# Optimization experiments

Measured on AMD Instinct MI355X. Metric: run time of the kernel, lower is better.

The kernel has to match this reference:

```python
import jax, jax.numpy as jnp
import numpy as np


def setup_inputs() -> dict:
    key = jax.random.key(0)
    k_x, k_w, k_W, k_b, k_idx = jax.random.split(key, 5)
    B, C, N, K, O = 2, 32, 40962, 25, 64
    x = jax.random.normal(k_x, (B, C, N), dtype=jnp.float32)
    neigh_weights = jax.random.uniform(k_w, (N, K, 3), dtype=jnp.float32)
    W = jax.random.normal(k_W, (O, K * C), dtype=jnp.float32) * 0.02
    b = jax.random.normal(k_b, (O,), dtype=jnp.float32) * 0.02
    neigh_indices = jax.random.randint(k_idx, (N, K, 3), 0, N, dtype=jnp.int32)
    return {"x": x, "neigh_weights": neigh_weights, "W": W, "b": b,
            "neigh_indices": neigh_indices}


def reference(x, neigh_weights, W, b, neigh_indices):
    # x: (B, C, N); neigh_indices/neigh_weights: (N, K, 3); W: (O, C*K); b: (O,)
    B, C, N = x.shape
    _, K, _ = neigh_indices.shape
    # Gather neighbor features: (B, C, N, K, 3)
    mat = x[:, :, neigh_indices]
    # Barycentric weighted sum over the 3 triangle vertices -> (B, C, N, K)
    s = jnp.einsum('bcnkt,nkt->bcnk', mat, neigh_weights)
    # Permute to (B, N, C, K) and apply Linear(C*K -> O)
    feat = s.transpose(0, 2, 1, 3).reshape(B * N, C * K)
    out = feat @ W.T + b  # (B*N, O)
    out = out.reshape(B, N, -1).transpose(0, 2, 1)  # (B, O, N)
    return out
```

## Files before the change

### kernel.cpp

```cpp
#include <hip/hip_runtime.h>
#include <hip/hip_fp16.h>

typedef __attribute__((ext_vector_type(8))) _Float16 half8;
typedef __attribute__((ext_vector_type(4))) float f32x4;

union U2H2 { unsigned int u; __half2 h; };

static __device__ __forceinline__ unsigned int pack2h(float a, float b) {
    U2H2 c; c.h = __floats2half2_rn(a, b); return c.u;
}
static __device__ __forceinline__ __half2 u_as_h2(unsigned int u) {
    U2H2 c; c.u = u; return c.h;
}
static __device__ __forceinline__ __half2 hi16(unsigned int u) {
    return u_as_h2(__builtin_amdgcn_perm(u, u, 0x03020302u));
}

#define SWZ(row, slot) \
    ((slot) ^ ((row) & 3) ^ (((row) >> 2) & 3) ^ (((row) >> 5) & 1))

#define LDS_BARRIER()                                                \
    do {                                                             \
        asm volatile("s_waitcnt lgkmcnt(0)" ::: "memory");           \
        __builtin_amdgcn_s_barrier();                                \
        __builtin_amdgcn_sched_barrier(0);                           \
    } while (0)

__global__ __launch_bounds__(256) void prep_all(const float* __restrict__ x,
                                                const float* __restrict__ W,
                                                unsigned short* __restrict__ xth,
                                                unsigned short* __restrict__ Wrh,
                                                int N, int nT) {
    int bid = blockIdx.x, tid = threadIdx.x;
    if (bid >= nT) {
        int k = bid - nT;
#pragma unroll
        for (int it = 0; it < 8; ++it) {
            int r = tid + 256 * it;
            int o = r >> 5, c = r & 31;
            __half h = __float2half(W[o * 800 + c * 25 + k]);
            Wrh[k * 2048 + r] = *reinterpret_cast<unsigned short*>(&h);
        }
        return;
    }
    __shared__ float t[2][32][65];
    int n0 = bid * 64;
#pragma unroll
    for (int i = 0; i < 16; ++i) {
        int e = tid + 256 * i;
        int b = e >> 11, c = (e >> 6) & 31, nl = e & 63;
        int n = n0 + nl;
        t[b][c][nl] = (n < N) ? x[(size_t)(b * 32 + c) * N + n] : 0.f;
    }
    __syncthreads();
    int nl = tid >> 2, q = tid & 3, n = n0 + nl;
    if (n < N) {
#pragma unroll
        for (int b = 0; b < 2; ++b) {
            uint4 p;
            p.x = pack2h(t[b][q * 8 + 0][nl], t[b][q * 8 + 1][nl]);
            p.y = pack2h(t[b][q * 8 + 2][nl], t[b][q * 8 + 3][nl]);
            p.z = pack2h(t[b][q * 8 + 4][nl], t[b][q * 8 + 5][nl]);
            p.w = pack2h(t[b][q * 8 + 6][nl], t[b][q * 8 + 7][nl]);
            *reinterpret_cast<uint4*>(xth + ((size_t)n * 64 + b * 32 + q * 8)) = p;
        }
    }
}

__global__ __launch_bounds__(256) void fused_main(
    const unsigned short* __restrict__ xth,
    const unsigned short* __restrict__ Wrh,
    const float* __restrict__ bias,
    const int* __restrict__ nidx,
    const float* __restrict__ nw,
    float* __restrict__ out,
    int N)
{
    __shared__ unsigned int idxw[32 * 104];
    __shared__ __align__(16) unsigned char sA[2][4096];
    __shared__ __align__(16) unsigned char sB[2][4096];

    const int tid = threadIdx.x;
    const int n0 = blockIdx.x * 32;

#pragma unroll
    for (int it = 0; it < 13; ++it) {
        int e = tid + 256 * it;
        if (e < 3328) idxw[e] = 0u;
    }
    __syncthreads();
#pragma unroll
    for (int it = 0; it < 10; ++it) {
        int e = tid + 256 * it;
        if (e < 2400) {
            int nl = e / 75, r = e - nl * 75;
            int kk = r / 3, t = r - kk * 3;
            int n = n0 + nl;
            unsigned int u = 0;
            if (n < N) {
                size_t s = (size_t)n0 * 75 + e;
                int j = nidx[s];
                __half hw = __float2half(nw[s]);
                u = (unsigned int)j |
                    ((unsigned int)*reinterpret_cast<unsigned short*>(&hw) << 16);
            }
            idxw[nl * 104 + kk * 4 + t] = u;
        }
    }
    __syncthreads();

    const int nl = tid >> 3;
    const int p8 = tid & 7;
    const int grow = (p8 >> 2) * 32 + nl;
    const int gq = p8 & 3;
    const int wr_off = grow * 64 + (SWZ(grow, gq) << 4);

    const int sbo = (tid >> 2) * 64 + (SWZ((tid >> 2), (tid & 3)) << 4);

    const int l = tid & 63, wv = tid >> 6, c16 = l & 15, g = l >> 4;
    const int arow = 16 * wv + c16;
    const int rd_a = arow * 64 + (SWZ(arow, g) << 4);

    const unsigned short* xg = xth + p8 * 8;
    const unsigned int* iprow = &idxw[nl * 104];

    unsigned int ru[3][3];
    uint4 rg[3][3];
    uint4 rB;

    f32x4 acc[4];
#pragma unroll
    for (int ot = 0; ot < 4; ++ot) acc[ot] = (f32x4){0.f, 0.f, 0.f, 0.f};

    rB = *reinterpret_cast<const uint4*>(Wrh + tid * 8);
#pragma unroll
    for (int kk = 0; kk < 3; ++kk) {
        uint4 iq = *reinterpret_cast<const uint4*>(iprow + kk * 4);
        ru[kk][0] = iq.x; ru[kk][1] = iq.y; ru[kk][2] = iq.z;
    }
#pragma unroll
    for (int kk = 0; kk < 3; ++kk)
#pragma unroll
        for (int t = 0; t < 3; ++t)
            rg[kk][t] = *reinterpret_cast<const uint4*>(xg + (ru[kk][t] & 0xffffu) * 64);

#pragma unroll
    for (int k = 0; k < 25; ++k) {
        const int gb = k % 3, buf = k & 1;

        *reinterpret_cast<uint4*>(&sB[buf][sbo]) = rB;
        if (k + 1 < 25)
            rB = *reinterpret_cast<const uint4*>(Wrh + (k + 1) * 2048 + tid * 8);

        {
            __half2 w0 = hi16(ru[gb][0]), w1 = hi16(ru[gb][1]), w2 = hi16(ru[gb][2]);
            uint4 v0 = rg[gb][0], v1 = rg[gb][1], v2 = rg[gb][2];
            uint4 pk; U2H2 c;
            c.h = __hfma2(u_as_h2(v0.x), w0, __hfma2(u_as_h2(v1.x), w1, __hmul2(u_as_h2(v2.x), w2)));
            pk.x = c.u;
            c.h = __hfma2(u_as_h2(v0.y), w0, __hfma2(u_as_h2(v1.y), w1, __hmul2(u_as_h2(v2.y), w2)));
            pk.y = c.u;
            c.h = __hfma2(u_as_h2(v0.z), w0, __hfma2(u_as_h2(v1.z), w1, __hmul2(u_as_h2(v2.z), w2)));
            pk.z = c.u;
            c.h = __hfma2(u_as_h2(v0.w), w0, __hfma2(u_as_h2(v1.w), w1, __hmul2(u_as_h2(v2.w), w2)));
            pk.w = c.u;
            *reinterpret_cast<uint4*>(&sA[buf][wr_off]) = pk;
        }

        uint4 niq;
        {
            int ka = (k + 3 < 25) ? k + 3 : 25;
            niq = *reinterpret_cast<const uint4*>(iprow + ka * 4);
        }

        LDS_BARRIER();

        if (k + 3 < 25) {
            ru[gb][0] = niq.x; ru[gb][1] = niq.y; ru[gb][2] = niq.z;
#pragma unroll
            for (int t = 0; t < 3; ++t)
                rg[gb][t] = *reinterpret_cast<const uint4*>(xg + (ru[gb][t] & 0xffffu) * 64);
        }

        {
            half8 af = *reinterpret_cast<const half8*>(&sA[buf][rd_a]);
#pragma unroll
            for (int ot = 0; ot < 4; ++ot) {
                int orow = ot * 16 + c16;
                half8 bf = *reinterpret_cast<const half8*>(
                    &sB[buf][orow * 64 + (SWZ(orow, g) << 4)]);
                acc[ot] = __builtin_amdgcn_mfma_f32_16x16x32_f16(af, bf, acc[ot], 0, 0, 0);
            }
        }
    }

#pragma unroll
    for (int ot = 0; ot < 4; ++ot) {
        int o = ot * 16 + c16;
        float bv = bias[o];
#pragma unroll
        for (int i = 0; i < 4; ++i) {
            int mrow = 16 * wv + 4 * g + i;
            int b = mrow >> 5, nn = n0 + (mrow & 31);
            if (nn < N) out[((size_t)b * 64 + o) * N + nn] = acc[ot][i] + bv;
        }
    }
}

extern "C" void kernel_launch(void* const* d_in, const int* in_sizes, int n_in,
                              void* d_out, int out_size, void* d_ws, size_t ws_size,
                              hipStream_t stream) {
    const float* x    = (const float*)d_in[0];
    const float* nw   = (const float*)d_in[1];
    const float* W    = (const float*)d_in[2];
    const float* bias = (const float*)d_in[3];
    const int*   nidx = (const int*)d_in[4];
    float* out = (float*)d_out;

    int N = in_sizes[0] / 64;

    unsigned short* xth = (unsigned short*)d_ws;
    unsigned short* Wrh = xth + (size_t)N * 64;

    int nT = (N + 63) / 64;
    prep_all<<<nT + 25, 256, 0, stream>>>(x, W, xth, Wrh, N, nT);

    fused_main<<<(N + 31) / 32, 256, 0, stream>>>(xth, Wrh, bias, nidx, nw, out, N);
}
```

Measured before the change: 58.14 us.

## Split fused gather+GEMM into separate gather and GEMM kernels via workspace

The fused kernel is split in two when the workspace is large enough. A gather kernel computes the barycentric-weighted neighbour features in fp16 and writes them to a K×N×64 intermediate buffer. A separate GEMM kernel then streams that buffer through LDS into MFMA, removing the index staging in LDS and the gather latency from the MFMA loop. The cost is roughly 130 MB of extra global write and read traffic plus one more launch.

After: 99.54 us. 1.71x slower.

```diff
diff --git a/kernel.cpp b/kernel.cpp
--- a/kernel.cpp
+++ b/kernel.cpp
@@ -63,6 +63,162 @@
             p.z = pack2h(t[b][q * 8 + 4][nl], t[b][q * 8 + 5][nl]);
             p.w = pack2h(t[b][q * 8 + 6][nl], t[b][q * 8 + 7][nl]);
             *reinterpret_cast<uint4*>(xth + ((size_t)n * 64 + b * 32 + q * 8)) = p;
+        }
+    }
+}
+
+__global__ __launch_bounds__(256) void gather_s(
+    const unsigned short* __restrict__ xth,
+    const int* __restrict__ nidx,
+    const float* __restrict__ nw,
+    unsigned short* __restrict__ s,
+    int N)
+{
+    const int tid = threadIdx.x;
+    const int n0 = blockIdx.x * 32;
+    const int nl = tid >> 3, p8 = tid & 7;
+    const int n = n0 + nl;
+    const int nc = (n < N) ? n : (N - 1);
+    const bool wr = (n < N);
+
+    const int*   ib = nidx + (size_t)nc * 75;
+    const float* wb = nw   + (size_t)nc * 75;
+    const unsigned short* xg = xth + p8 * 8;
+
+    int3   ri[2];
+    float3 rw[2];
+    unsigned int rwh[2][3];
+    uint4  rg[2][3];
+
+    {
+        int3 i0 = *reinterpret_cast<const int3*>(ib + 0);
+        float3 w0 = *reinterpret_cast<const float3*>(wb + 0);
+        int3 i1 = *reinterpret_cast<const int3*>(ib + 3);
+        float3 w1 = *reinterpret_cast<const float3*>(wb + 3);
+        rg[0][0] = *reinterpret_cast<const uint4*>(xg + i0.x * 64);
+        rg[0][1] = *reinterpret_cast<const uint4*>(xg + i0.y * 64);
+        rg[0][2] = *reinterpret_cast<const uint4*>(xg + i0.z * 64);
+        rg[1][0] = *reinterpret_cast<const uint4*>(xg + i1.x * 64);
+        rg[1][1] = *reinterpret_cast<const uint4*>(xg + i1.y * 64);
+        rg[1][2] = *reinterpret_cast<const uint4*>(xg + i1.z * 64);
+        rwh[0][0] = pack2h(w0.x, w0.x); rwh[0][1] = pack2h(w0.y, w0.y);
+        rwh[0][2] = pack2h(w0.z, w0.z);
+        rwh[1][0] = pack2h(w1.x, w1.x); rwh[1][1] = pack2h(w1.y, w1.y);
+        rwh[1][2] = pack2h(w1.z, w1.z);
+        ri[0] = *reinterpret_cast<const int3*>(ib + 6);
+        rw[0] = *reinterpret_cast<const float3*>(wb + 6);
+        ri[1] = *reinterpret_cast<const int3*>(ib + 9);
+        rw[1] = *reinterpret_cast<const float3*>(wb + 9);
+    }
+
+#pragma unroll
+    for (int k = 0; k < 25; ++k) {
+        const int gb = k & 1;
+
+        __half2 w0 = u_as_h2(rwh[gb][0]), w1 = u_as_h2(rwh[gb][1]),
+                w2 = u_as_h2(rwh[gb][2]);
+        uint4 v0 = rg[gb][0], v1 = rg[gb][1], v2 = rg[gb][2];
+        uint4 pk; U2H2 c;
+        c.h = __hfma2(u_as_h2(v0.x), w0, __hfma2(u_as_h2(v1.x), w1, __hmul2(u_as_h2(v2.x), w2)));
+        pk.x = c.u;
+        c.h = __hfma2(u_as_h2(v0.y), w0, __hfma2(u_as_h2(v1.y), w1, __hmul2(u_as_h2(v2.y), w2)));
+        pk.y = c.u;
+        c.h = __hfma2(u_as_h2(v0.z), w0, __hfma2(u_as_h2(v1.z), w1, __hmul2(u_as_h2(v2.z), w2)));
+        pk.z = c.u;
+        c.h = __hfma2(u_as_h2(v0.w), w0, __hfma2(u_as_h2(v1.w), w1, __hmul2(u_as_h2(v2.w), w2)));
+        pk.w = c.u;
+        if (wr)
+            *reinterpret_cast<uint4*>(s + ((size_t)k * N + n) * 64 + p8 * 8) = pk;
+
+        if (k + 2 < 25) {
+            rg[gb][0] = *reinterpret_cast<const uint4*>(xg + ri[gb].x * 64);
+            rg[gb][1] = *reinterpret_cast<const uint4*>(xg + ri[gb].y * 64);
+            rg[gb][2] = *reinterpret_cast<const uint4*>(xg + ri[gb].z * 64);
+            rwh[gb][0] = pack2h(rw[gb].x, rw[gb].x);
+            rwh[gb][1] = pack2h(rw[gb].y, rw[gb].y);
+            rwh[gb][2] = pack2h(rw[gb].z, rw[gb].z);
+            int ka = (k + 4 <= 24) ? k + 4 : 24;
+            ri[gb] = *reinterpret_cast<const int3*>(ib + ka * 3);
+            rw[gb] = *reinterpret_cast<const float3*>(wb + ka * 3);
+        }
+    }
+}
+
+__global__ __launch_bounds__(256) void gemm_s(
+    const unsigned short* __restrict__ s,
+    const unsigned short* __restrict__ Wrh,
+    const float* __restrict__ bias,
+    float* __restrict__ out,
+    int N)
+{
+    __shared__ __align__(16) unsigned char sA[2][4096];
+    __shared__ __align__(16) unsigned char sB[2][4096];
+
+    const int tid = threadIdx.x;
+    const int n0 = blockIdx.x * 32;
+
+    const int nl = tid >> 3, p8 = tid & 7;
+    const int grow = (p8 >> 2) * 32 + nl;
+    const int gq = p8 & 3;
+    const int wr_off = grow * 64 + (SWZ(grow, gq) << 4);
+
+    const int sbo = (tid >> 2) * 64 + (SWZ((tid >> 2), (tid & 3)) << 4);
+
+    const int l = tid & 63, wv = tid >> 6, c16 = l & 15, g = l >> 4;
+    const int arow = 16 * wv + c16;
+    const int rd_a = arow * 64 + (SWZ(arow, g) << 4);
+
+    const int nc = (n0 + nl < N) ? (n0 + nl) : (N - 1);
+    const unsigned short* sp = s + (size_t)nc * 64 + p8 * 8;
+
+    uint4 rs[3];
+    uint4 rB;
+
+    f32x4 acc[4];
+#pragma unroll
+    for (int ot = 0; ot < 4; ++ot) acc[ot] = (f32x4){0.f, 0.f, 0.f, 0.f};
+
+    rB = *reinterpret_cast<const uint4*>(Wrh + tid * 8);
+    rs[0] = *reinterpret_cast<const uint4*>(sp + (size_t)0 * N * 64);
+    rs[1] = *reinterpret_cast<const uint4*>(sp + (size_t)1 * N * 64);
+    rs[2] = *reinterpret_cast<const uint4*>(sp + (size_t)2 * N * 64);
+
+#pragma unroll
+    for (int k = 0; k < 25; ++k) {
+        const int sb = k % 3, buf = k & 1;
+
+        *reinterpret_cast<uint4*>(&sB[buf][sbo]) = rB;
+        if (k + 1 < 25)
+            rB = *reinterpret_cast<const uint4*>(Wrh + (k + 1) * 2048 + tid * 8);
+
+        *reinterpret_cast<uint4*>(&sA[buf][wr_off]) = rs[sb];
+
+        LDS_BARRIER();
+
+        if (k + 3 < 25)
+            rs[sb] = *reinterpret_cast<const uint4*>(sp + (size_t)(k + 3) * N * 64);
+
+        {
+            half8 af = *reinterpret_cast<const half8*>(&sA[buf][rd_a]);
+#pragma unroll
+            for (int ot = 0; ot < 4; ++ot) {
+                int orow = ot * 16 + c16;
+                half8 bf = *reinterpret_cast<const half8*>(
+                    &sB[buf][orow * 64 + (SWZ(orow, g) << 4)]);
+                acc[ot] = __builtin_amdgcn_mfma_f32_16x16x32_f16(af, bf, acc[ot], 0, 0, 0);
+            }
+        }
+    }
+
+#pragma unroll
+    for (int ot = 0; ot < 4; ++ot) {
+        int o = ot * 16 + c16;
+        float bv = bias[o];
+#pragma unroll
+        for (int i = 0; i < 4; ++i) {
+            int mrow = 16 * wv + 4 * g + i;
+            int b = mrow >> 5, nn = n0 + (mrow & 31);
+            if (nn < N) out[((size_t)b * 64 + o) * N + nn] = acc[ot][i] + bv;
         }
     }
 }
@@ -98,9 +254,9 @@
             int n = n0 + nl;
             unsigned int u = 0;
             if (n < N) {
-                size_t s = (size_t)n0 * 75 + e;
-                int j = nidx[s];
-                __half hw = __float2half(nw[s]);
+                size_t ss = (size_t)n0 * 75 + e;
+                int j = nidx[ss];
+                __half hw = __float2half(nw[ss]);
                 u = (unsigned int)j |
                     ((unsigned int)*reinterpret_cast<unsigned short*>(&hw) << 16);
             }
@@ -114,7 +270,6 @@
     const int grow = (p8 >> 2) * 32 + nl;
     const int gq = p8 & 3;
     const int wr_off = grow * 64 + (SWZ(grow, gq) << 4);
-
     const int sbo = (tid >> 2) * 64 + (SWZ((tid >> 2), (tid & 3)) << 4);
 
     const int l = tid & 63, wv = tid >> 6, c16 = l & 15, g = l >> 4;
@@ -221,9 +376,19 @@
 
     unsigned short* xth = (unsigned short*)d_ws;
     unsigned short* Wrh = xth + (size_t)N * 64;
+    unsigned short* s   = Wrh + 51200;
+
+    size_t need = ((size_t)N * 64 + 51200 + (size_t)N * 25 * 64 + 2048)
+                  * sizeof(unsigned short);
 
     int nT = (N + 63) / 64;
     prep_all<<<nT + 25, 256, 0, stream>>>(x, W, xth, Wrh, N, nT);
 
-    fused_main<<<(N + 31) / 32, 256, 0, stream>>>(xth, Wrh, bias, nidx, nw, out, N);
-}
+    int nblk = (N + 31) / 32;
+    if (ws_size >= need) {
+        gather_s<<<nblk, 256, 0, stream>>>(xth, nidx, nw, s, N);
+        gemm_s<<<nblk, 256, 0, stream>>>(s, Wrh, bias, out, N);
+    } else {
+        fused_main<<<nblk, 256, 0, stream>>>(xth, Wrh, bias, nidx, nw, out, N);
+    }
+}
```
